# Kernel tuning notes

Measured on AMD Instinct MI355X. Metric: run time of the kernel, lower is better.

The kernel has to match this reference:

```python
import jax, jax.numpy as jnp
import numpy as np

B, L, C = 32, 64, 4


def setup_inputs() -> dict:
    key = jax.random.key(0)
    k_idx, k0, k1, k2, k3 = jax.random.split(key, 5)
    # One-hot encoded sequences, flattened to (B, L*C) as the layer expects.
    idx = jax.random.randint(k_idx, (B, L), 0, C)
    x_lc = jax.nn.one_hot(idx, C, dtype=jnp.float32).reshape(B, L * C)
    return {
        "x_lc": x_lc,
        "theta_0": jnp.zeros((1,), dtype=jnp.float32),  # Constant(0.0) init
        "theta_1": 0.05 * jax.random.normal(k1, (L, C), dtype=jnp.float32),
        "theta_2": 0.05 * jax.random.normal(k2, (L, C, L, C), dtype=jnp.float32),
        "theta_3": 0.05 * jax.random.normal(k3, (L, C, L, C, L, C), dtype=jnp.float32),
    }


def reference(x_lc, theta_0, theta_1, theta_2, theta_3):
    Lp, Cp = theta_1.shape
    xr = x_lc.reshape(-1, Lp, Cp)  # (B, L, C)
    pos = jnp.arange(Lp)
    # strict upper-triangular position masks: l0 < l1 (< l2)
    m2 = (pos[None, :] > pos[:, None]).astype(theta_2.dtype)      # (L, L)
    m3 = m2[:, :, None] * m2[None, :, :]                           # (L, L, L)
    # order 1: sum_{l,c} theta_1[l,c] x[b,l,c]
    phi = theta_0[0] + jnp.einsum('ua,bua->b', theta_1, xr)
    # order 2: sum over l0<l1 of theta_2 * x x
    phi = phi + jnp.einsum('uavc,uv,bua,bvc->b', theta_2, m2, xr, xr)
    # order 3: sum over l0<l1<l2 of theta_3 * x x x
    phi = phi + jnp.einsum('uavcwe,uvw,bua,bvc,bwe->b', theta_3, m3, xr, xr, xr)
    return phi.reshape(-1, 1)
```

## Files before the change

kernel.cpp:

```cpp
#include <hip/hip_runtime.h>

#define BB 32
#define LL 64
#define CC 4
#define LC (LL * CC)
#define NPAIR (LL * (LL - 1) / 2)

__global__ __launch_bounds__(256) void setup_kernel(
    const float* __restrict__ x, float* __restrict__ out, int* __restrict__ p)
{
    int gid = blockIdx.x * 256 + threadIdx.x;
    if (gid < BB * LL) {
        int b = gid >> 6;
        int l = gid & 63;
        const float* xr = x + b * LC + l * CC;
        int c = 0;
        float best = xr[0];
#pragma unroll
        for (int k = 1; k < CC; ++k) {
            float v = xr[k];
            if (v > best) { best = v; c = k; }
        }
        p[gid] = l * CC + c;
    }
    if (gid < BB) out[gid] = 0.0f;
}

__global__ __launch_bounds__(256) void main_kernel(
    const float* __restrict__ t0, const float* __restrict__ t1,
    const float* __restrict__ t2, const float* __restrict__ t3,
    const int* __restrict__ p, float* __restrict__ out)
{
    const int b = blockIdx.x;
    const int tid = threadIdx.x;

    __shared__ int sp[LL];
    if (tid < LL) sp[tid] = p[b * LL + tid];
    __syncthreads();

    float acc = 0.0f;
    int t = blockIdx.y * 256 + tid;
    if (t < NPAIR) {
        int v = (int)((1.0f + sqrtf(8.0f * (float)t + 1.0f)) * 0.5f);
        while (v * (v - 1) / 2 > t) --v;
        while ((v + 1) * v / 2 <= t) ++v;
        int u = t - v * (v - 1) / 2;

        int pu = sp[u];
        int pv = sp[v];
        acc = t2[pu * LC + pv];

        const float* __restrict__ t3row = t3 + (size_t)pu * (LC * LC) + pv * LC;
        for (int w = v + 1; w < LL; ++w) {
            acc += t3row[sp[w]];
        }
    }
    if (blockIdx.y == 0) {
        if (tid < LL) acc += t1[sp[tid]];
        if (tid == 0) acc += t0[0];
    }

    for (int off = 32; off > 0; off >>= 1) acc += __shfl_down(acc, off, 64);
    __shared__ float wsum[4];
    if ((tid & 63) == 0) wsum[tid >> 6] = acc;
    __syncthreads();
    if (tid == 0) atomicAdd(&out[b], wsum[0] + wsum[1] + wsum[2] + wsum[3]);
}

extern "C" void kernel_launch(void* const* d_in, const int* in_sizes, int n_in,
                              void* d_out, int out_size, void* d_ws, size_t ws_size,
                              hipStream_t stream) {
    const float* x  = (const float*)d_in[0];
    const float* t0 = (const float*)d_in[1];
    const float* t1 = (const float*)d_in[2];
    const float* t2 = (const float*)d_in[3];
    const float* t3 = (const float*)d_in[4];
    float* out = (float*)d_out;
    int* p = (int*)d_ws;

    setup_kernel<<<(BB * LL + 255) / 256, 256, 0, stream>>>(x, out, p);
    main_kernel<<<dim3(BB, 8), 256, 0, stream>>>(t0, t1, t2, t3, p, out);
}
```

Before: 120.3 us.

## Split pair tasks in halves, balance chunks, fold setup into main kernel

Moves the one-hot argmax into the main kernel and removes the setup launch. Each (u,v) pair's inner w-loop is split into two half-tasks. Chunks are paired front-to-back within a block so triangular work is balanced across blocks. The t3 row is read as float4 with per-element channel selection, and the atomic accumulation is replaced by per-block partial sums plus a small deterministic reduce kernel. This aims to cut load imbalance and serial loop length, at the cost of reading four times more t3 bytes per w and adding a second launch.

```diff
diff --git a/kernel.cpp b/kernel.cpp
--- a/kernel.cpp
+++ b/kernel.cpp
@@ -3,68 +3,82 @@
 #define BB 32
 #define LL 64
 #define CC 4
-#define LC (LL * CC)
-#define NPAIR (LL * (LL - 1) / 2)
-
-__global__ __launch_bounds__(256) void setup_kernel(
-    const float* __restrict__ x, float* __restrict__ out, int* __restrict__ p)
-{
-    int gid = blockIdx.x * 256 + threadIdx.x;
-    if (gid < BB * LL) {
-        int b = gid >> 6;
-        int l = gid & 63;
-        const float* xr = x + b * LC + l * CC;
-        int c = 0;
-        float best = xr[0];
-#pragma unroll
-        for (int k = 1; k < CC; ++k) {
-            float v = xr[k];
-            if (v > best) { best = v; c = k; }
-        }
-        p[gid] = l * CC + c;
-    }
-    if (gid < BB) out[gid] = 0.0f;
-}
+#define LC 256
+#define NPAIR 2016
+#define NTASK 4032
+#define CHUNK 126
+#define NCHUNK 32
+#define YBLK 16
 
 __global__ __launch_bounds__(256) void main_kernel(
+    const float* __restrict__ x,
     const float* __restrict__ t0, const float* __restrict__ t1,
     const float* __restrict__ t2, const float* __restrict__ t3,
-    const int* __restrict__ p, float* __restrict__ out)
+    float* __restrict__ ws)
 {
     const int b = blockIdx.x;
+    const int y = blockIdx.y;
     const int tid = threadIdx.x;
 
     __shared__ int sp[LL];
-    if (tid < LL) sp[tid] = p[b * LL + tid];
+    if (tid < LL) {
+        const float* xr = x + b * LC + tid * CC;
+        int c = 0; float best = xr[0];
+#pragma unroll
+        for (int k = 1; k < CC; ++k) { float v = xr[k]; if (v > best) { best = v; c = k; } }
+        sp[tid] = tid * CC + c;
+    }
     __syncthreads();
 
     float acc = 0.0f;
-    int t = blockIdx.y * 256 + tid;
-    if (t < NPAIR) {
+    const int lane = tid & 127;
+    const int chunk = (tid < 128) ? y : (NCHUNK - 1 - y);
+    if (lane < CHUNK) {
+        int s = chunk * CHUNK + lane;
+        int t = s >> 1;
+        int h = s & 1;
         int v = (int)((1.0f + sqrtf(8.0f * (float)t + 1.0f)) * 0.5f);
         while (v * (v - 1) / 2 > t) --v;
         while ((v + 1) * v / 2 <= t) ++v;
         int u = t - v * (v - 1) / 2;
 
-        int pu = sp[u];
-        int pv = sp[v];
-        acc = t2[pu * LC + pv];
+        int pu = sp[u], pv = sp[v];
+        int n = 63 - v;
+        int half1 = (n + 1) >> 1;
+        int wlo = v + 1 + (h ? half1 : 0);
+        int whi = h ? 64 : (v + 1 + half1);
+        if (h == 0) acc += t2[pu * LC + pv];
 
-        const float* __restrict__ t3row = t3 + (size_t)pu * (LC * LC) + pv * LC;
-        for (int w = v + 1; w < LL; ++w) {
-            acc += t3row[sp[w]];
+        const float4* __restrict__ row =
+            (const float4*)(t3 + (size_t)pu * (LC * LC) + (size_t)pv * LC);
+#pragma unroll 4
+        for (int w = wlo; w < whi; ++w) {
+            float4 f = row[w];
+            int c = sp[w] & 3;
+            acc += (c == 0) ? f.x : (c == 1) ? f.y : (c == 2) ? f.z : f.w;
         }
     }
-    if (blockIdx.y == 0) {
-        if (tid < LL) acc += t1[sp[tid]];
-        if (tid == 0) acc += t0[0];
+    if (y == 0 && tid >= 128 && tid < 192) {
+        acc += t1[sp[tid - 128]];
+        if (tid == 128) acc += t0[0];
     }
 
     for (int off = 32; off > 0; off >>= 1) acc += __shfl_down(acc, off, 64);
     __shared__ float wsum[4];
     if ((tid & 63) == 0) wsum[tid >> 6] = acc;
     __syncthreads();
-    if (tid == 0) atomicAdd(&out[b], wsum[0] + wsum[1] + wsum[2] + wsum[3]);
+    if (tid == 0) ws[b * YBLK + y] = wsum[0] + wsum[1] + wsum[2] + wsum[3];
+}
+
+__global__ __launch_bounds__(512) void reduce_kernel(
+    const float* __restrict__ ws, float* __restrict__ out)
+{
+    int tid = threadIdx.x;
+    int b = tid >> 4, slot = tid & 15;
+    float v = ws[b * YBLK + slot];
+#pragma unroll
+    for (int off = 8; off > 0; off >>= 1) v += __shfl_down(v, off, 16);
+    if (slot == 0) out[b] = v;
 }
 
 extern "C" void kernel_launch(void* const* d_in, const int* in_sizes, int n_in,
@@ -76,8 +90,8 @@
     const float* t2 = (const float*)d_in[3];
     const float* t3 = (const float*)d_in[4];
     float* out = (float*)d_out;
-    int* p = (int*)d_ws;
+    float* ws = (float*)d_ws;
 
-    setup_kernel<<<(BB * LL + 255) / 256, 256, 0, stream>>>(x, out, p);
-    main_kernel<<<dim3(BB, 8), 256, 0, stream>>>(t0, t1, t2, t3, p, out);
+    main_kernel<<<dim3(BB, YBLK), 256, 0, stream>>>(x, t0, t1, t2, t3, ws);
+    reduce_kernel<<<1, 512, 0, stream>>>(ws, out);
 }
```

Measured after the change: 110.6 us. -8.0%, faster.

## Parallelize over (u,v) pairs across batch with deterministic two-stage reduction

Applied to the files above, without the earlier changes.

Launches one block per (u,v) position pair, covering all 32 batch rows with 8 threads each. Each block recomputes the one-hot argmax indices into shared memory and strides over w, so threads for different batches read the same t3 region. Per-pair partial sums go to a workspace, and a single-block reduce kernel sums them and adds the order-0 and order-1 terms. This replaces the atomic accumulation and the separate setup kernel, at the cost of redundant argmax work in every block and a serial one-block final reduction.

```diff
diff --git a/kernel.cpp b/kernel.cpp
--- a/kernel.cpp
+++ b/kernel.cpp
@@ -2,69 +2,79 @@
 
 #define BB 32
 #define LL 64
-#define CC 4
-#define LC (LL * CC)
-#define NPAIR (LL * (LL - 1) / 2)
+#define LC 256
+#define NPAIR 2016
+#define SPS 72
+#define WSTRIDE 2048
 
-__global__ __launch_bounds__(256) void setup_kernel(
-    const float* __restrict__ x, float* __restrict__ out, int* __restrict__ p)
+__global__ __launch_bounds__(256) void pair_kernel(
+    const float* __restrict__ x, const float* __restrict__ t2,
+    const float* __restrict__ t3, float* __restrict__ ws)
 {
-    int gid = blockIdx.x * 256 + threadIdx.x;
-    if (gid < BB * LL) {
-        int b = gid >> 6;
-        int l = gid & 63;
-        const float* xr = x + b * LC + l * CC;
-        int c = 0;
-        float best = xr[0];
+    const int t = blockIdx.x;
+    const int tid = threadIdx.x;
+
+    int v = (int)((1.0f + sqrtf(8.0f * (float)t + 1.0f)) * 0.5f);
+    while (v * (v - 1) / 2 > t) --v;
+    while ((v + 1) * v / 2 <= t) ++v;
+    const int u = t - v * (v - 1) / 2;
+
+    __shared__ short sp[BB * SPS];
+    {
+        const float4* __restrict__ x4 = (const float4*)x;
 #pragma unroll
-        for (int k = 1; k < CC; ++k) {
-            float v = xr[k];
-            if (v > best) { best = v; c = k; }
+        for (int i = 0; i < 8; ++i) {
+            int idx = i * 256 + tid;
+            float4 f = x4[idx];
+            int c = 0; float best = f.x;
+            if (f.y > best) { best = f.y; c = 1; }
+            if (f.z > best) { best = f.z; c = 2; }
+            if (f.w > best) { best = f.w; c = 3; }
+            sp[(idx >> 6) * SPS + (idx & 63)] = (short)(((idx & 63) << 2) | c);
         }
-        p[gid] = l * CC + c;
     }
-    if (gid < BB) out[gid] = 0.0f;
+    __syncthreads();
+
+    const int b = tid >> 3, k = tid & 7;
+    const short* __restrict__ spb = sp + b * SPS;
+    const int pu = spb[u], pv = spb[v];
+    const float* __restrict__ row = t3 + ((size_t)pu << 16) + ((size_t)pv << 8);
+
+    float acc = 0.0f;
+    for (int w = v + 1 + k; w < LL; w += 8)
+        acc += row[spb[w]];
+
+    acc += __shfl_down(acc, 4, 8);
+    acc += __shfl_down(acc, 2, 8);
+    acc += __shfl_down(acc, 1, 8);
+    if (k == 0) ws[b * WSTRIDE + t] = acc + t2[pu * LC + pv];
 }
 
-__global__ __launch_bounds__(256) void main_kernel(
-    const float* __restrict__ t0, const float* __restrict__ t1,
-    const float* __restrict__ t2, const float* __restrict__ t3,
-    const int* __restrict__ p, float* __restrict__ out)
+__global__ __launch_bounds__(1024) void reduce_kernel(
+    const float* __restrict__ x, const float* __restrict__ t0,
+    const float* __restrict__ t1, const float* __restrict__ ws,
+    float* __restrict__ out)
 {
-    const int b = blockIdx.x;
     const int tid = threadIdx.x;
+    const int b = tid >> 5, j = tid & 31;
+    const float* __restrict__ wsb = ws + b * WSTRIDE;
+    float v = 0.0f;
+    for (int t = j; t < NPAIR; t += 32) v += wsb[t];
 
-    __shared__ int sp[LL];
-    if (tid < LL) sp[tid] = p[b * LL + tid];
-    __syncthreads();
-
-    float acc = 0.0f;
-    int t = blockIdx.y * 256 + tid;
-    if (t < NPAIR) {
-        int v = (int)((1.0f + sqrtf(8.0f * (float)t + 1.0f)) * 0.5f);
-        while (v * (v - 1) / 2 > t) --v;
-        while ((v + 1) * v / 2 <= t) ++v;
-        int u = t - v * (v - 1) / 2;
-
-        int pu = sp[u];
-        int pv = sp[v];
-        acc = t2[pu * LC + pv];
-
-        const float* __restrict__ t3row = t3 + (size_t)pu * (LC * LC) + pv * LC;
-        for (int w = v + 1; w < LL; ++w) {
-            acc += t3row[sp[w]];
-        }
-    }
-    if (blockIdx.y == 0) {
-        if (tid < LL) acc += t1[sp[tid]];
-        if (tid == 0) acc += t0[0];
+    const float4* __restrict__ x4 = (const float4*)x;
+#pragma unroll
+    for (int i = 0; i < 2; ++i) {
+        int w = j + i * 32;
+        float4 f = x4[b * 64 + w];
+        int c = 0; float best = f.x;
+        if (f.y > best) { best = f.y; c = 1; }
+        if (f.z > best) { best = f.z; c = 2; }
+        if (f.w > best) { best = f.w; c = 3; }
+        v += t1[(w << 2) | c];
     }
 
-    for (int off = 32; off > 0; off >>= 1) acc += __shfl_down(acc, off, 64);
-    __shared__ float wsum[4];
-    if ((tid & 63) == 0) wsum[tid >> 6] = acc;
-    __syncthreads();
-    if (tid == 0) atomicAdd(&out[b], wsum[0] + wsum[1] + wsum[2] + wsum[3]);
+    for (int off = 16; off > 0; off >>= 1) v += __shfl_down(v, off, 32);
+    if (j == 0) out[b] = v + t0[0];
 }
 
 extern "C" void kernel_launch(void* const* d_in, const int* in_sizes, int n_in,
@@ -76,8 +86,8 @@
     const float* t2 = (const float*)d_in[3];
     const float* t3 = (const float*)d_in[4];
     float* out = (float*)d_out;
-    int* p = (int*)d_ws;
+    float* ws = (float*)d_ws;
 
-    setup_kernel<<<(BB * LL + 255) / 256, 256, 0, stream>>>(x, out, p);
-    main_kernel<<<dim3(BB, 8), 256, 0, stream>>>(t0, t1, t2, t3, p, out);
+    pair_kernel<<<NPAIR, 256, 0, stream>>>(x, t2, t3, ws);
+    reduce_kernel<<<1, 1024, 0, stream>>>(x, t0, t1, ws, out);
 }
```

Result: no change. 119.5 us (-0.6%).
